# Kernel optimization log

Hardware: AMD Instinct MI355X
Metric: run time of the kernel (lower is better)

Reference implementation:

```python
import jax, jax.numpy as jnp
import numpy as np

F_DIM, H, O = 128, 256, 256
NQ, EQ = 64, 512
ND, ED = 50000, 600000

PARAM_SHAPES = [
    ("qW1", (F_DIM, H)), ("qb1", (H,)), ("qW2", (H, H)), ("qb2", (H,)),
    ("qW3", (H, H)),     ("qb3", (H,)), ("qW4", (H, O)), ("qb4", (O,)),
    ("dW1", (F_DIM, H)), ("db1", (H,)), ("dW2", (H, H)), ("db2", (H,)),
    ("dW3", (H, H)),     ("db3", (H,)), ("dW4", (H, O)), ("db4", (O,)),
    ("lW1", (2 * O, O)), ("lb1", (O,)),
    ("lW2", (O, O // 2)), ("lb2", (O // 2,)),
    ("lW3", (O // 2, 8)), ("lb3", (8,)),
]

def setup_inputs() -> dict:
    key = jax.random.key(0)
    ks = jax.random.split(key, 4 + len(PARAM_SHAPES))
    inp = {
        "query_in_feat": jax.random.normal(ks[0], (NQ, F_DIM), jnp.float32),
        "data_in_feat": jax.random.normal(ks[1], (ND, F_DIM), jnp.float32),
        "query_edge_list": jax.random.randint(ks[2], (2, EQ), 0, NQ),
        "data_edge_list": jax.random.randint(ks[3], (2, ED), 0, ND),
    }
    for i, (name, shape) in enumerate(PARAM_SHAPES):
        fan_in = shape[0] if len(shape) == 2 else 1
        inp[name] = jax.random.normal(ks[4 + i], shape, jnp.float32) * (1.0 / np.sqrt(fan_in))
    return inp

def _mlp2(x, W1, b1, W2, b2):
    return jnp.maximum(x @ W1 + b1, 0.0) @ W2 + b2

def _gin_conv(x, src, dst, W1, b1, W2, b2):
    # GINConv (eps=0): MLP(x_i + sum_{j->i} x_j); gather x[src], scatter-add at dst
    agg = jax.ops.segment_sum(x[src], dst, num_segments=x.shape[0])
    return _mlp2(x + agg, W1, b1, W2, b2)

def _gin(x, edge_index, p):
    src, dst = edge_index[0], edge_index[1]
    h = jnp.maximum(_gin_conv(x, src, dst, *p[:4]), 0.0)  # ReLU between convs
    return _gin_conv(h, src, dst, *p[4:])

def reference(query_in_feat, data_in_feat, query_edge_list, data_edge_list,
              qW1, qb1, qW2, qb2, qW3, qb3, qW4, qb4,
              dW1, db1, dW2, db2, dW3, db3, dW4, db4,
              lW1, lb1, lW2, lb2, lW3, lb3):
    qx = _gin(query_in_feat, query_edge_list, (qW1, qb1, qW2, qb2, qW3, qb3, qW4, qb4))
    dx = _gin(data_in_feat, data_edge_list, (dW1, db1, dW2, db2, dW3, db3, dW4, db4))
    # global_add_pool with batch = zeros -> single-graph sum
    qp = jnp.sum(qx, axis=0, keepdims=True)  # [1, O]
    dp = jnp.sum(dx, axis=0, keepdims=True)  # [1, O]
    h = jnp.concatenate([qp, dp], axis=1)    # [1, 2*O]
    h = jnp.maximum(h @ lW1 + lb1, 0.0)
    h = jnp.maximum(h @ lW2 + lb2, 0.0)
    h = jnp.maximum(h @ lW3 + lb3, 0.0)
    return h.reshape(1, 8)
```

## Files before the change

kernel.cpp:

```cpp
#include <hip/hip_runtime.h>
#include <hip/hip_bf16.h>


#define NQ 64
#define EQ 512
#define ND 50000
#define ED 600000
#define FDIM 128
#define HDIM 256
#define MLP_GRID 512

typedef __attribute__((ext_vector_type(8))) short short8;
typedef __attribute__((ext_vector_type(4))) float f32x4;
typedef __attribute__((ext_vector_type(2))) float floatx2;
typedef __attribute__((ext_vector_type(4))) unsigned short us4;
typedef __attribute__((ext_vector_type(2))) unsigned short us2;

__device__ __forceinline__ unsigned short f2bf(float f) {
    union { float f; unsigned u; } v; v.f = f;
    unsigned r = v.u + 0x7FFF + ((v.u >> 16) & 1);
    return (unsigned short)(r >> 16);
}
__device__ __forceinline__ float bf2f(unsigned short u) {
    union { unsigned u; float f; } v; v.u = ((unsigned)u) << 16;
    return v.f;
}


struct PackDesc {
    const float* W[8];
    unsigned short* Wp[8];
    int KT[8];
    int start[9];
};

__device__ __forceinline__ void pack_unit(const PackDesc& pd, int unit, int l) {
    int m = 0;
    while (m < 7 && unit >= pd.start[m + 1]) ++m;
    const int local = unit - pd.start[m];
    const int KT = pd.KT[m];
    const int kt = local % KT;
    const int ct = local / KT;
    const float* W = pd.W[m];
    unsigned short* Wp = pd.Wp[m];
    const int row = kt * 32 + (l >> 4) * 8;
    const int col = ct * 16 + (l & 15);
    short8 v;
#pragma unroll
    for (int j = 0; j < 8; ++j) v[j] = (short)f2bf(W[(size_t)(row + j) * 256 + col]);
    *(short8*)(Wp + (((size_t)(ct * KT + kt)) * 64 + l) * 8) = v;
}


__global__ void prepass(const float* __restrict__ xd, const float* __restrict__ xq,
                        unsigned char* __restrict__ x8, long long nd4, long long n4,
                        int cvt_b, PackDesc pd, int pack_units, int pack_b,
                        const int* __restrict__ d_dst, int* __restrict__ d_deg,
                        const int* __restrict__ q_dst, int* __restrict__ q_deg,
                        int d_eb) {
    const int b = blockIdx.x;
    const int tid = threadIdx.x;
    if (b < cvt_b) {
        long long i = (long long)b * 256 + tid;
        if (i >= n4) return;
        const float* src = (i < nd4) ? (xd + i * 4) : (xq + (i - nd4) * 4);
        float4 v = *(const float4*)src;
        int p = __builtin_amdgcn_cvt_pk_fp8_f32(v.x, v.y, 0, false);
        p = __builtin_amdgcn_cvt_pk_fp8_f32(v.z, v.w, p, true);
        *(unsigned*)(x8 + i * 4) = (unsigned)p;
    } else if (b < cvt_b + pack_b) {
        const int unit = (b - cvt_b) * 4 + (tid >> 6);
        if (unit < pack_units) pack_unit(pd, unit, tid & 63);
    } else {
        const int cb = b - cvt_b - pack_b;
        if (cb < d_eb) {
            int e = cb * 256 + tid;
            if (e < ED) atomicAdd(&d_deg[d_dst[e]], 1);
        } else {
            int e = (cb - d_eb) * 256 + tid;
            if (e < EQ) atomicAdd(&q_deg[q_dst[e]], 1);
        }
    }
}


__device__ __forceinline__ void scan1_body(const int* deg, int* rowptr, int* bsum,
                                           int n, int blk) {
    __shared__ int sh[256];
    const int t = threadIdx.x;
    const int i = blk * 256 + t;
    const int v = (i < n) ? deg[i] : 0;
    sh[t] = v;
    __syncthreads();
    for (int off = 1; off < 256; off <<= 1) {
        int x = (t >= off) ? sh[t - off] : 0;
        __syncthreads();
        sh[t] += x;
        __syncthreads();
    }
    if (i < n) rowptr[i] = sh[t] - v;
    if (t == 255) bsum[blk] = sh[255];
}

__global__ void scan_phase1_both(const int* __restrict__ d_deg, int* __restrict__ d_rowptr,
                                 int* __restrict__ d_bsum,
                                 const int* __restrict__ q_deg, int* __restrict__ q_rowptr,
                                 int* __restrict__ q_bsum, int dblocks) {
    int b = blockIdx.x;
    if (b < dblocks) scan1_body(d_deg, d_rowptr, d_bsum, ND, b);
    else             scan1_body(q_deg, q_rowptr, q_bsum, NQ, b - dblocks);
}

__device__ __forceinline__ void scan2_body(const int* bsum, int* boff, int* rowptr_n, int nb) {
    __shared__ int sh[256];
    const int t = threadIdx.x;
    const int v = (t < nb) ? bsum[t] : 0;
    sh[t] = v;
    __syncthreads();
    for (int off = 1; off < 256; off <<= 1) {
        int x = (t >= off) ? sh[t - off] : 0;
        __syncthreads();
        sh[t] += x;
        __syncthreads();
    }
    if (t < nb) boff[t] = sh[t] - v;
    if (t == 255) *rowptr_n = sh[255];
}

__global__ void scan_phase2_both(const int* __restrict__ d_bsum, int* __restrict__ d_boff,
                                 int* __restrict__ d_rowptr_n, int d_nb,
                                 const int* __restrict__ q_bsum, int* __restrict__ q_boff,
                                 int* __restrict__ q_rowptr_n, int q_nb) {
    if (blockIdx.x == 0) scan2_body(d_bsum, d_boff, d_rowptr_n, d_nb);
    else                 scan2_body(q_bsum, q_boff, q_rowptr_n, q_nb);
}

__global__ void scan_phase3_both(int* __restrict__ d_rowptr, const int* __restrict__ d_boff,
                                 int* __restrict__ d_cursor,
                                 int* __restrict__ q_rowptr, const int* __restrict__ q_boff,
                                 int* __restrict__ q_cursor, int dblocks) {
    int b = blockIdx.x;
    if (b < dblocks) {
        int i = b * 256 + threadIdx.x;
        if (i < ND) {
            int r = d_rowptr[i] + d_boff[b];
            d_rowptr[i] = r; d_cursor[i] = r;
        }
    } else {
        int i = (b - dblocks) * 256 + threadIdx.x;
        if (i < NQ) {
            int r = q_rowptr[i] + q_boff[b - dblocks];
            q_rowptr[i] = r; q_cursor[i] = r;
        }
    }
}

__global__ void fill_csr_both(const int* __restrict__ d_src, const int* __restrict__ d_dst,
                              int* __restrict__ d_cursor, int* __restrict__ d_csrsrc,
                              const int* __restrict__ q_src, const int* __restrict__ q_dst,
                              int* __restrict__ q_cursor, int* __restrict__ q_csrsrc,
                              int dblocks) {
    int b = blockIdx.x;
    if (b < dblocks) {
        int e = b * 256 + threadIdx.x;
        if (e < ED) {
            int p = atomicAdd(&d_cursor[d_dst[e]], 1);
            d_csrsrc[p] = d_src[e];
        }
    } else {
        int e = (b - dblocks) * 256 + threadIdx.x;
        if (e < EQ) {
            int p = atomicAdd(&q_cursor[q_dst[e]], 1);
            q_csrsrc[p] = q_src[e];
        }
    }
}


__global__ void gin_agg_f8_128_dual(const unsigned char* __restrict__ xd,
                                    const int* __restrict__ rpd, const int* __restrict__ csd,
                                    unsigned short* __restrict__ od,
                                    const unsigned char* __restrict__ xq,
                                    const int* __restrict__ rpq, const int* __restrict__ csq,
                                    unsigned short* __restrict__ oq, int ndpair) {
    const unsigned char* x; const int* rowptr; const int* csr; unsigned short* out; int nb;
    if ((int)blockIdx.x < ndpair) { x = xd; rowptr = rpd; csr = csd; out = od; nb = blockIdx.x; }
    else { x = xq; rowptr = rpq; csr = csq; out = oq; nb = blockIdx.x - ndpair; }

    const int t = threadIdx.x;
    const int node = nb * 2 + (t >> 5);
    const int c = t & 31;

    const int beg = rowptr[node];
    const int end = rowptr[node + 1];

    float a0, a1, a2, a3;
    {
        const unsigned w = *(const unsigned*)(x + (size_t)node * 128 + c * 4);
        floatx2 lo = __builtin_amdgcn_cvt_pk_f32_fp8((int)w, false);
        floatx2 hi = __builtin_amdgcn_cvt_pk_f32_fp8((int)w, true);
        a0 = lo[0]; a1 = lo[1]; a2 = hi[0]; a3 = hi[1];
    }
    for (int j = beg; j < end; ++j) {
        const unsigned w = *(const unsigned*)(x + (size_t)csr[j] * 128 + c * 4);
        floatx2 lo = __builtin_amdgcn_cvt_pk_f32_fp8((int)w, false);
        floatx2 hi = __builtin_amdgcn_cvt_pk_f32_fp8((int)w, true);
        a0 += lo[0]; a1 += lo[1]; a2 += hi[0]; a3 += hi[1];
    }
    us4 r;
    r[0] = f2bf(a0); r[1] = f2bf(a1); r[2] = f2bf(a2); r[3] = f2bf(a3);
    *(us4*)(out + (size_t)node * 128 + c * 4) = r;
}


__global__ void gin_agg_f8_256_dual(const unsigned char* __restrict__ xd,
                                    const int* __restrict__ rpd, const int* __restrict__ csd,
                                    unsigned short* __restrict__ od,
                                    const unsigned char* __restrict__ xq,
                                    const int* __restrict__ rpq, const int* __restrict__ csq,
                                    unsigned short* __restrict__ oq) {
    const unsigned char* x; const int* rowptr; const int* csr; unsigned short* out; int node;
    if ((int)blockIdx.x < ND) { x = xd; rowptr = rpd; csr = csd; out = od; node = blockIdx.x; }
    else { x = xq; rowptr = rpq; csr = csq; out = oq; node = blockIdx.x - ND; }

    const int t = threadIdx.x;
    const int beg = rowptr[node];
    const int end = rowptr[node + 1];

    float a0, a1, a2, a3;
    {
        const unsigned w = *(const unsigned*)(x + (size_t)node * 256 + t * 4);
        floatx2 lo = __builtin_amdgcn_cvt_pk_f32_fp8((int)w, false);
        floatx2 hi = __builtin_amdgcn_cvt_pk_f32_fp8((int)w, true);
        a0 = lo[0]; a1 = lo[1]; a2 = hi[0]; a3 = hi[1];
    }
    int j = beg;
    for (; j + 1 < end; j += 2) {
        const unsigned w0 = *(const unsigned*)(x + (size_t)csr[j] * 256 + t * 4);
        const unsigned w1 = *(const unsigned*)(x + (size_t)csr[j + 1] * 256 + t * 4);
        floatx2 l0 = __builtin_amdgcn_cvt_pk_f32_fp8((int)w0, false);
        floatx2 h0 = __builtin_amdgcn_cvt_pk_f32_fp8((int)w0, true);
        floatx2 l1 = __builtin_amdgcn_cvt_pk_f32_fp8((int)w1, false);
        floatx2 h1 = __builtin_amdgcn_cvt_pk_f32_fp8((int)w1, true);
        a0 += l0[0] + l1[0]; a1 += l0[1] + l1[1];
        a2 += h0[0] + h1[0]; a3 += h0[1] + h1[1];
    }
    if (j < end) {
        const unsigned w0 = *(const unsigned*)(x + (size_t)csr[j] * 256 + t * 4);
        floatx2 l0 = __builtin_amdgcn_cvt_pk_f32_fp8((int)w0, false);
        floatx2 h0 = __builtin_amdgcn_cvt_pk_f32_fp8((int)w0, true);
        a0 += l0[0]; a1 += l0[1]; a2 += h0[0]; a3 += h0[1];
    }
    us4 r;
    r[0] = f2bf(a0); r[1] = f2bf(a1); r[2] = f2bf(a2); r[3] = f2bf(a3);
    *(us4*)(out + (size_t)node * 256 + t * 4) = r;
}


template <int KIN>
__global__ __launch_bounds__(256) void mlp_dual(
    const unsigned short* __restrict__ Ad,
    const unsigned short* __restrict__ W1pd, const float* __restrict__ b1d,
    const unsigned short* __restrict__ W2pd, const float* __restrict__ b2d,
    unsigned char* __restrict__ C8d, float* __restrict__ poold, int ndtiles,
    const unsigned short* __restrict__ Aq,
    const unsigned short* __restrict__ W1pq, const float* __restrict__ b1q,
    const unsigned short* __restrict__ W2pq, const float* __restrict__ b2q,
    unsigned char* __restrict__ C8q, float* __restrict__ poolq,
    int relu_out, int total_tiles) {
    constexpr int KT1 = KIN / 32;
    constexpr int ISSUES = KIN / 32;
    constexpr int LPR = KIN / 8;
    constexpr int RPC = 1024 / (2 * KIN);
    __shared__ __align__(16) unsigned short lds[2][64 * 256];

    const int tid = threadIdx.x;
    const int lane = tid & 63;
    const int wv = tid >> 6;
    const int lrow = lane & 15;
    const int lk2 = (lane >> 4) * 8;

    const int nt = (total_tiles - (int)blockIdx.x + MLP_GRID - 1) / MLP_GRID;
    if (nt <= 0) return;

    const int rc = lane / LPR;
    const int cc = lane % LPR;

    auto STAGE = [&](int bu, int g) {
        const unsigned short* Abase =
            (g < ndtiles) ? (Ad + (size_t)g * 64 * KIN) : (Aq + (size_t)(g - ndtiles) * 64 * KIN);
#pragma unroll
        for (int i = 0; i < ISSUES; ++i) {
            const int chunk = wv * ISSUES + i;
            const int r = chunk * RPC + rc;
            const char* src = (const char*)Abase + (size_t)r * (2 * KIN) + ((cc ^ (r & 7)) << 4);
            __builtin_amdgcn_global_load_lds(src, (char*)&lds[bu][0] + chunk * 1024, 16, 0, 0);
        }
    };

    STAGE(0, (int)blockIdx.x);
    int cur = 0;

    for (int t = 0; t < nt; ++t) {
        const int g = (int)blockIdx.x + t * MLP_GRID;
        const unsigned short *W1p, *W2p; const float *b1, *b2;
        unsigned char* C8; float* pool; int row0, N;
        if (g < ndtiles) {
            W1p = W1pd; b1 = b1d; W2p = W2pd; b2 = b2d; C8 = C8d; pool = poold;
            row0 = g * 64; N = ND;
        } else {
            W1p = W1pq; b1 = b1q; W2p = W2pq; b2 = b2q; C8 = C8q; pool = poolq;
            row0 = (g - ndtiles) * 64; N = NQ;
        }

        __syncthreads();
        if (t + 1 < nt) STAGE(cur ^ 1, (int)blockIdx.x + (t + 1) * MLP_GRID);

        unsigned short* buf = &lds[cur][0];

        f32x4 acc1[4][4];
#pragma unroll
        for (int fm = 0; fm < 4; ++fm)
#pragma unroll
            for (int fn = 0; fn < 4; ++fn) acc1[fm][fn] = (f32x4)(0.f);

        const unsigned short* W1Base = W1p + ((size_t)(wv * 4) * KT1 * 64 + lane) * 8;
        for (int kt = 0; kt < KT1; ++kt) {
            short8 a[4], bf[4];
#pragma unroll
            for (int fm = 0; fm < 4; ++fm) {
                const int r = fm * 16 + lrow;
                unsigned byte = (unsigned)((r * KIN + kt * 32 + lk2) * 2) ^ (unsigned)((r & 7) << 4);
                a[fm] = *(const short8*)((const char*)buf + byte);
            }
#pragma unroll
            for (int fn = 0; fn < 4; ++fn)
                bf[fn] = *(const short8*)(W1Base + ((size_t)fn * KT1 + kt) * 64 * 8);
#pragma unroll
            for (int fm = 0; fm < 4; ++fm)
#pragma unroll
                for (int fn = 0; fn < 4; ++fn)
                    acc1[fm][fn] = __builtin_amdgcn_mfma_f32_16x16x32_bf16(
                        a[fm], bf[fn], acc1[fm][fn], 0, 0, 0);
        }
        __syncthreads();

#pragma unroll
        for (int fn = 0; fn < 4; ++fn) {
            const int col = wv * 64 + fn * 16 + lrow;
            const float bv = b1[col];
#pragma unroll
            for (int fm = 0; fm < 4; ++fm) {
                const int rbase = fm * 16 + (lane >> 4) * 4;
#pragma unroll
                for (int r = 0; r < 4; ++r) {
                    const int row = rbase + r;
                    const float v = fmaxf(acc1[fm][fn][r] + bv, 0.f);
                    unsigned byte = (unsigned)((row * 256 + col) * 2) ^ (unsigned)((row & 7) << 4);
                    *(unsigned short*)((char*)buf + byte) = f2bf(v);
                }
            }
        }
        __syncthreads();

        f32x4 acc2[4][4];
#pragma unroll
        for (int fm = 0; fm < 4; ++fm)
#pragma unroll
            for (int fn = 0; fn < 4; ++fn) acc2[fm][fn] = (f32x4)(0.f);

        const unsigned short* W2Base = W2p + ((size_t)(wv * 4) * 8 * 64 + lane) * 8;
        for (int kt = 0; kt < 8; ++kt) {
            short8 a[4], bf[4];
#pragma unroll
            for (int fm = 0; fm < 4; ++fm) {
                const int r = fm * 16 + lrow;
                unsigned byte = (unsigned)((r * 256 + kt * 32 + lk2) * 2) ^ (unsigned)((r & 7) << 4);
                a[fm] = *(const short8*)((const char*)buf + byte);
            }
#pragma unroll
            for (int fn = 0; fn < 4; ++fn)
                bf[fn] = *(const short8*)(W2Base + ((size_t)fn * 8 + kt) * 64 * 8);
#pragma unroll
            for (int fm = 0; fm < 4; ++fm)
#pragma unroll
                for (int fn = 0; fn < 4; ++fn)
                    acc2[fm][fn] = __builtin_amdgcn_mfma_f32_16x16x32_bf16(
                        a[fm], bf[fn], acc2[fm][fn], 0, 0, 0);
        }

#pragma unroll
        for (int fn = 0; fn < 4; ++fn) {
            const int col = wv * 64 + fn * 16 + lrow;
            const float bv = b2[col];
            float ps = 0.f;
#pragma unroll
            for (int fm = 0; fm < 4; ++fm) {
                const int rbase = row0 + fm * 16 + (lane >> 4) * 4;
#pragma unroll
                for (int r = 0; r < 4; ++r) {
                    const int row = rbase + r;
                    if (row < N) {
                        float v = acc2[fm][fn][r] + bv;
                        if (relu_out) v = fmaxf(v, 0.f);
                        if (C8) {
                            unsigned p = (unsigned)__builtin_amdgcn_cvt_pk_fp8_f32(v, v, 0, false);
                            C8[(size_t)row * 256 + col] = (unsigned char)(p & 0xff);
                        }
                        ps += v;
                    }
                }
            }
            if (pool) {
                ps += __shfl_xor(ps, 16);
                ps += __shfl_xor(ps, 32);
                if ((lane >> 4) == 0) atomicAdd(&pool[col], ps);
            }
        }
        cur ^= 1;
    }
}


__global__ void mlp_head(const float* __restrict__ pooled,
                         const float* __restrict__ lW1, const float* __restrict__ lb1,
                         const float* __restrict__ lW2, const float* __restrict__ lb2,
                         const float* __restrict__ lW3, const float* __restrict__ lb3,
                         float* __restrict__ out) {
    __shared__ float h0[512];
    __shared__ float h1[256];
    __shared__ float h2[128];
    const int t = threadIdx.x;
    h0[t] = pooled[t];
    h0[t + 256] = pooled[t + 256];
    __syncthreads();

    float acc = lb1[t];
    for (int k = 0; k < 512; ++k) acc += h0[k] * lW1[k * 256 + t];
    h1[t] = fmaxf(acc, 0.f);
    __syncthreads();

    if (t < 128) {
        float a = lb2[t];
        for (int k = 0; k < 256; ++k) a += h1[k] * lW2[k * 128 + t];
        h2[t] = fmaxf(a, 0.f);
    }
    __syncthreads();

    if (t < 8) {
        float a = lb3[t];
        for (int k = 0; k < 128; ++k) a += h2[k] * lW3[k * 8 + t];
        out[t] = fmaxf(a, 0.f);
    }
}


extern "C" void kernel_launch(void* const* d_in, const int* in_sizes, int n_in,
                              void* d_out, int out_size, void* d_ws, size_t ws_size,
                              hipStream_t stream) {
    const float* q_x  = (const float*)d_in[0];
    const float* d_x  = (const float*)d_in[1];
    const int*   q_el = (const int*)d_in[2];
    const int*   d_el = (const int*)d_in[3];
    const float* qW1 = (const float*)d_in[4];  const float* qb1 = (const float*)d_in[5];
    const float* qW2 = (const float*)d_in[6];  const float* qb2 = (const float*)d_in[7];
    const float* qW3 = (const float*)d_in[8];  const float* qb3 = (const float*)d_in[9];
    const float* qW4 = (const float*)d_in[10]; const float* qb4 = (const float*)d_in[11];
    const float* dW1 = (const float*)d_in[12]; const float* db1 = (const float*)d_in[13];
    const float* dW2 = (const float*)d_in[14]; const float* db2 = (const float*)d_in[15];
    const float* dW3 = (const float*)d_in[16]; const float* db3 = (const float*)d_in[17];
    const float* dW4 = (const float*)d_in[18]; const float* db4 = (const float*)d_in[19];
    const float* lW1 = (const float*)d_in[20]; const float* lb1 = (const float*)d_in[21];
    const float* lW2 = (const float*)d_in[22]; const float* lb2 = (const float*)d_in[23];
    const float* lW3 = (const float*)d_in[24]; const float* lb3 = (const float*)d_in[25];
    (void)in_sizes; (void)n_in; (void)out_size; (void)ws_size;

    const int* q_src = q_el;  const int* q_dst = q_el + EQ;
    const int* d_src = d_el;  const int* d_dst = d_el + ED;

    char* wsb = (char*)d_ws;
    size_t off = 0;
    auto alloc = [&](size_t bytes) { void* p = wsb + off; off += (bytes + 255) & ~(size_t)255; return p; };

    unsigned char*  x8d = (unsigned char*)alloc((size_t)ND * FDIM);
    unsigned char*  x8q = (unsigned char*)alloc((size_t)NQ * FDIM);
    unsigned short* dag = (unsigned short*)alloc((size_t)ND * FDIM * 2);
    unsigned short* qag = (unsigned short*)alloc((size_t)NQ * FDIM * 2);
    unsigned char*  h8d = (unsigned char*)alloc((size_t)ND * HDIM);
    unsigned char*  h8q = (unsigned char*)alloc((size_t)NQ * HDIM);
    unsigned short* had = (unsigned short*)alloc((size_t)ND * HDIM * 2);
    unsigned short* haq = (unsigned short*)alloc((size_t)NQ * HDIM * 2);
    float* pooled = (float*)alloc(512 * 4);
    int* d_deg    = (int*)alloc((size_t)ND * 4);
    int* q_deg    = (int*)alloc((size_t)NQ * 4);
    int* d_rowptr = (int*)alloc((size_t)(ND + 1) * 4);
    int* d_cursor = (int*)alloc((size_t)ND * 4);
    int* d_csrsrc = (int*)alloc((size_t)ED * 4);
    int* d_bsum   = (int*)alloc(256 * 4);
    int* d_boff   = (int*)alloc(256 * 4);
    int* q_rowptr = (int*)alloc((size_t)(NQ + 1) * 4);
    int* q_cursor = (int*)alloc((size_t)NQ * 4);
    int* q_csrsrc = (int*)alloc((size_t)EQ * 4);
    int* q_bsum   = (int*)alloc(256 * 4);
    int* q_boff   = (int*)alloc(256 * 4);
    unsigned short* pdW1 = (unsigned short*)alloc((size_t)FDIM * 256 * 2);
    unsigned short* pdW2 = (unsigned short*)alloc((size_t)HDIM * 256 * 2);
    unsigned short* pdW3 = (unsigned short*)alloc((size_t)HDIM * 256 * 2);
    unsigned short* pdW4 = (unsigned short*)alloc((size_t)HDIM * 256 * 2);
    unsigned short* pqW1 = (unsigned short*)alloc((size_t)FDIM * 256 * 2);
    unsigned short* pqW2 = (unsigned short*)alloc((size_t)HDIM * 256 * 2);
    unsigned short* pqW3 = (unsigned short*)alloc((size_t)HDIM * 256 * 2);
    unsigned short* pqW4 = (unsigned short*)alloc((size_t)HDIM * 256 * 2);

    hipMemsetAsync(pooled, 0, 512 * 4, stream);
    hipMemsetAsync(d_deg, 0, (char*)(q_deg + NQ) - (char*)d_deg, stream);

    const int d_eb = (ED + 255) / 256;
    const int q_eb = (EQ + 255) / 256;
    const int d_nb = (ND + 255) / 256;
    const int q_nb = (NQ + 255) / 256;
    {
        PackDesc pd;
        const float* Ws[8] = {dW1, dW2, dW3, dW4, qW1, qW2, qW3, qW4};
        unsigned short* Wps[8] = {pdW1, pdW2, pdW3, pdW4, pqW1, pqW2, pqW3, pqW4};
        int kts[8] = {4, 8, 8, 8, 4, 8, 8, 8};
        int s = 0;
        for (int i = 0; i < 8; ++i) {
            pd.W[i] = Ws[i]; pd.Wp[i] = Wps[i]; pd.KT[i] = kts[i];
            pd.start[i] = s; s += 16 * kts[i];
        }
        pd.start[8] = s;
        const int pack_units = s;
        const int pack_b = (s + 3) / 4;
        long long nd4 = (long long)ND * FDIM / 4;
        long long n4 = nd4 + (long long)NQ * FDIM / 4;
        const int cvt_b = (int)((n4 + 255) / 256);
        prepass<<<cvt_b + pack_b + d_eb + q_eb, 256, 0, stream>>>(
            d_x, q_x, x8d, nd4, n4, cvt_b, pd, pack_units, pack_b,
            d_dst, d_deg, q_dst, q_deg, d_eb);
    }

    scan_phase1_both<<<d_nb + q_nb, 256, 0, stream>>>(d_deg, d_rowptr, d_bsum,
                                                      q_deg, q_rowptr, q_bsum, d_nb);
    scan_phase2_both<<<2, 256, 0, stream>>>(d_bsum, d_boff, d_rowptr + ND, d_nb,
                                            q_bsum, q_boff, q_rowptr + NQ, q_nb);
    scan_phase3_both<<<d_nb + q_nb, 256, 0, stream>>>(d_rowptr, d_boff, d_cursor,
                                                      q_rowptr, q_boff, q_cursor, d_nb);
    fill_csr_both<<<d_eb + q_eb, 256, 0, stream>>>(d_src, d_dst, d_cursor, d_csrsrc,
                                                   q_src, q_dst, q_cursor, q_csrsrc, d_eb);

    const int ndpair = ND / 2;
    const int qpair = NQ / 2;
    const int ndtiles = (ND + 63) / 64;
    const int total_tiles = ndtiles + 1;

    gin_agg_f8_128_dual<<<ndpair + qpair, 64, 0, stream>>>(
        x8d, d_rowptr, d_csrsrc, dag, x8q, q_rowptr, q_csrsrc, qag, ndpair);
    mlp_dual<FDIM><<<MLP_GRID, 256, 0, stream>>>(
        dag, pdW1, db1, pdW2, db2, h8d, nullptr, ndtiles,
        qag, pqW1, qb1, pqW2, qb2, h8q, nullptr, 1, total_tiles);

    gin_agg_f8_256_dual<<<ND + NQ, 64, 0, stream>>>(
        h8d, d_rowptr, d_csrsrc, had, h8q, q_rowptr, q_csrsrc, haq);
    mlp_dual<HDIM><<<MLP_GRID, 256, 0, stream>>>(
        had, pdW3, db3, pdW4, db4, nullptr, pooled + 256, ndtiles,
        haq, pqW3, qb3, pqW4, qb4, nullptr, pooled, 0, total_tiles);

    mlp_head<<<1, 256, 0, stream>>>(pooled, lW1, lb1, lW2, lb2, lW3, lb3, (float*)d_out);
}
```

Before: 272.5 us.

## Split MLP into per-wave 16-row tiles with LDS pool reduction

Replaces the persistent 64-row-tile, double-buffered MLP kernel with a one-shot grid in which each wave independently processes a 16-row tile across all 256 output columns. The block-wide __syncthreads barriers between the two GEMM stages go away, and occupancy rises with launch_bounds(256,4) and a smaller LDS footprint. Pooled sums are reduced in shared memory before a single global atomic per column per block. In exchange, each wave streams the full weight matrices from cache for only 16 rows, so weight reuse per load drops about fourfold and global/L2 weight traffic grows. Prefetch overlap of the next tile is also lost.

```diff
diff --git a/kernel.cpp b/kernel.cpp
--- a/kernel.cpp
+++ b/kernel.cpp
@@ -8,7 +8,6 @@
 #define ED 600000
 #define FDIM 128
 #define HDIM 256
-#define MLP_GRID 512
 
 typedef __attribute__((ext_vector_type(8))) short short8;
 typedef __attribute__((ext_vector_type(4))) float f32x4;
@@ -258,11 +257,11 @@
 
 
 template <int KIN>
-__global__ __launch_bounds__(256) void mlp_dual(
+__global__ __launch_bounds__(256, 4) void mlp_dual(
     const unsigned short* __restrict__ Ad,
     const unsigned short* __restrict__ W1pd, const float* __restrict__ b1d,
     const unsigned short* __restrict__ W2pd, const float* __restrict__ b2d,
-    unsigned char* __restrict__ C8d, float* __restrict__ poold, int ndtiles,
+    unsigned char* __restrict__ C8d, float* __restrict__ poold, int ndt,
     const unsigned short* __restrict__ Aq,
     const unsigned short* __restrict__ W1pq, const float* __restrict__ b1q,
     const unsigned short* __restrict__ W2pq, const float* __restrict__ b2q,
@@ -272,7 +271,8 @@
     constexpr int ISSUES = KIN / 32;
     constexpr int LPR = KIN / 8;
     constexpr int RPC = 1024 / (2 * KIN);
-    __shared__ __align__(16) unsigned short lds[2][64 * 256];
+    __shared__ __align__(16) unsigned short lds[4][16 * 256];
+    __shared__ float poolsh[2][256];
 
     const int tid = threadIdx.x;
     const int lane = tid & 63;
@@ -280,144 +280,115 @@
     const int lrow = lane & 15;
     const int lk2 = (lane >> 4) * 8;
 
-    const int nt = (total_tiles - (int)blockIdx.x + MLP_GRID - 1) / MLP_GRID;
-    if (nt <= 0) return;
-
-    const int rc = lane / LPR;
-    const int cc = lane % LPR;
-
-    auto STAGE = [&](int bu, int g) {
-        const unsigned short* Abase =
-            (g < ndtiles) ? (Ad + (size_t)g * 64 * KIN) : (Aq + (size_t)(g - ndtiles) * 64 * KIN);
-#pragma unroll
-        for (int i = 0; i < ISSUES; ++i) {
-            const int chunk = wv * ISSUES + i;
-            const int r = chunk * RPC + rc;
-            const char* src = (const char*)Abase + (size_t)r * (2 * KIN) + ((cc ^ (r & 7)) << 4);
-            __builtin_amdgcn_global_load_lds(src, (char*)&lds[bu][0] + chunk * 1024, 16, 0, 0);
-        }
-    };
-
-    STAGE(0, (int)blockIdx.x);
-    int cur = 0;
-
-    for (int t = 0; t < nt; ++t) {
-        const int g = (int)blockIdx.x + t * MLP_GRID;
-        const unsigned short *W1p, *W2p; const float *b1, *b2;
-        unsigned char* C8; float* pool; int row0, N;
-        if (g < ndtiles) {
-            W1p = W1pd; b1 = b1d; W2p = W2pd; b2 = b2d; C8 = C8d; pool = poold;
-            row0 = g * 64; N = ND;
+    const bool do_pool = (poold != nullptr) || (poolq != nullptr);
+    if (do_pool) {
+        ((float*)poolsh)[tid] = 0.f;
+        ((float*)poolsh)[tid + 256] = 0.f;
+        __syncthreads();
+    }
+
+    const int g = (int)blockIdx.x * 4 + wv;
+    if (g < total_tiles) {
+        const unsigned short *A, *W1p, *W2p; const float *b1, *b2;
+        unsigned char* C8; int row0, graph;
+        if (g < ndt) {
+            A = Ad; W1p = W1pd; b1 = b1d; W2p = W2pd; b2 = b2d; C8 = C8d;
+            graph = 0; row0 = g * 16;
         } else {
-            W1p = W1pq; b1 = b1q; W2p = W2pq; b2 = b2q; C8 = C8q; pool = poolq;
-            row0 = (g - ndtiles) * 64; N = NQ;
-        }
-
-        __syncthreads();
-        if (t + 1 < nt) STAGE(cur ^ 1, (int)blockIdx.x + (t + 1) * MLP_GRID);
-
-        unsigned short* buf = &lds[cur][0];
-
-        f32x4 acc1[4][4];
-#pragma unroll
-        for (int fm = 0; fm < 4; ++fm)
-#pragma unroll
-            for (int fn = 0; fn < 4; ++fn) acc1[fm][fn] = (f32x4)(0.f);
-
-        const unsigned short* W1Base = W1p + ((size_t)(wv * 4) * KT1 * 64 + lane) * 8;
+            A = Aq; W1p = W1pq; b1 = b1q; W2p = W2pq; b2 = b2q; C8 = C8q;
+            graph = 1; row0 = (g - ndt) * 16;
+        }
+        unsigned short* slice = &lds[wv][0];
+
+        {
+            const char* Abase = (const char*)A + (size_t)row0 * KIN * 2;
+            const int rl = lane / LPR;
+            const int cc = lane % LPR;
+#pragma unroll
+            for (int i = 0; i < ISSUES; ++i) {
+                const int r = i * RPC + rl;
+                const char* src = Abase + (size_t)r * (2 * KIN) + ((size_t)(cc ^ (r & 7)) << 4);
+                __builtin_amdgcn_global_load_lds(src, (char*)slice + i * 1024, 16, 0, 0);
+            }
+        }
+        asm volatile("s_waitcnt vmcnt(0)" ::: "memory");
+
+        f32x4 acc1[16];
+#pragma unroll
+        for (int fn = 0; fn < 16; ++fn) acc1[fn] = (f32x4)(0.f);
+
         for (int kt = 0; kt < KT1; ++kt) {
-            short8 a[4], bf[4];
-#pragma unroll
-            for (int fm = 0; fm < 4; ++fm) {
-                const int r = fm * 16 + lrow;
-                unsigned byte = (unsigned)((r * KIN + kt * 32 + lk2) * 2) ^ (unsigned)((r & 7) << 4);
-                a[fm] = *(const short8*)((const char*)buf + byte);
+            const unsigned byte =
+                (unsigned)((lrow * KIN + kt * 32 + lk2) * 2) ^ (unsigned)((lrow & 7) << 4);
+            const short8 a = *(const short8*)((const char*)slice + byte);
+#pragma unroll
+            for (int fn = 0; fn < 16; ++fn) {
+                const short8 bf = *(const short8*)(W1p + (((size_t)(fn * KT1 + kt)) * 64 + lane) * 8);
+                acc1[fn] = __builtin_amdgcn_mfma_f32_16x16x32_bf16(a, bf, acc1[fn], 0, 0, 0);
             }
-#pragma unroll
-            for (int fn = 0; fn < 4; ++fn)
-                bf[fn] = *(const short8*)(W1Base + ((size_t)fn * KT1 + kt) * 64 * 8);
-#pragma unroll
-            for (int fm = 0; fm < 4; ++fm)
-#pragma unroll
-                for (int fn = 0; fn < 4; ++fn)
-                    acc1[fm][fn] = __builtin_amdgcn_mfma_f32_16x16x32_bf16(
-                        a[fm], bf[fn], acc1[fm][fn], 0, 0, 0);
-        }
-        __syncthreads();
-
-#pragma unroll
-        for (int fn = 0; fn < 4; ++fn) {
-            const int col = wv * 64 + fn * 16 + lrow;
+        }
+
+#pragma unroll
+        for (int fn = 0; fn < 16; ++fn) {
+            const int col = fn * 16 + lrow;
             const float bv = b1[col];
 #pragma unroll
-            for (int fm = 0; fm < 4; ++fm) {
-                const int rbase = fm * 16 + (lane >> 4) * 4;
-#pragma unroll
-                for (int r = 0; r < 4; ++r) {
-                    const int row = rbase + r;
-                    const float v = fmaxf(acc1[fm][fn][r] + bv, 0.f);
-                    unsigned byte = (unsigned)((row * 256 + col) * 2) ^ (unsigned)((row & 7) << 4);
-                    *(unsigned short*)((char*)buf + byte) = f2bf(v);
-                }
+            for (int r = 0; r < 4; ++r) {
+                const int row = (lane >> 4) * 4 + r;
+                const float v = fmaxf(acc1[fn][r] + bv, 0.f);
+                const unsigned byte =
+                    (unsigned)((row * 256 + col) * 2) ^ (unsigned)((row & 7) << 4);
+                *(unsigned short*)((char*)slice + byte) = f2bf(v);
             }
         }
-        __syncthreads();
-
-        f32x4 acc2[4][4];
-#pragma unroll
-        for (int fm = 0; fm < 4; ++fm)
-#pragma unroll
-            for (int fn = 0; fn < 4; ++fn) acc2[fm][fn] = (f32x4)(0.f);
-
-        const unsigned short* W2Base = W2p + ((size_t)(wv * 4) * 8 * 64 + lane) * 8;
+
+        f32x4 acc2[16];
+#pragma unroll
+        for (int fn = 0; fn < 16; ++fn) acc2[fn] = (f32x4)(0.f);
+
         for (int kt = 0; kt < 8; ++kt) {
-            short8 a[4], bf[4];
-#pragma unroll
-            for (int fm = 0; fm < 4; ++fm) {
-                const int r = fm * 16 + lrow;
-                unsigned byte = (unsigned)((r * 256 + kt * 32 + lk2) * 2) ^ (unsigned)((r & 7) << 4);
-                a[fm] = *(const short8*)((const char*)buf + byte);
+            const unsigned byte =
+                (unsigned)((lrow * 256 + kt * 32 + lk2) * 2) ^ (unsigned)((lrow & 7) << 4);
+            const short8 a = *(const short8*)((const char*)slice + byte);
+#pragma unroll
+            for (int fn = 0; fn < 16; ++fn) {
+                const short8 bf = *(const short8*)(W2p + (((size_t)(fn * 8 + kt)) * 64 + lane) * 8);
+                acc2[fn] = __builtin_amdgcn_mfma_f32_16x16x32_bf16(a, bf, acc2[fn], 0, 0, 0);
             }
-#pragma unroll
-            for (int fn = 0; fn < 4; ++fn)
-                bf[fn] = *(const short8*)(W2Base + ((size_t)fn * 8 + kt) * 64 * 8);
-#pragma unroll
-            for (int fm = 0; fm < 4; ++fm)
-#pragma unroll
-                for (int fn = 0; fn < 4; ++fn)
-                    acc2[fm][fn] = __builtin_amdgcn_mfma_f32_16x16x32_bf16(
-                        a[fm], bf[fn], acc2[fm][fn], 0, 0, 0);
-        }
-
-#pragma unroll
-        for (int fn = 0; fn < 4; ++fn) {
-            const int col = wv * 64 + fn * 16 + lrow;
+        }
+
+#pragma unroll
+        for (int fn = 0; fn < 16; ++fn) {
+            const int col = fn * 16 + lrow;
             const float bv = b2[col];
             float ps = 0.f;
 #pragma unroll
-            for (int fm = 0; fm < 4; ++fm) {
-                const int rbase = row0 + fm * 16 + (lane >> 4) * 4;
-#pragma unroll
-                for (int r = 0; r < 4; ++r) {
-                    const int row = rbase + r;
-                    if (row < N) {
-                        float v = acc2[fm][fn][r] + bv;
-                        if (relu_out) v = fmaxf(v, 0.f);
-                        if (C8) {
-                            unsigned p = (unsigned)__builtin_amdgcn_cvt_pk_fp8_f32(v, v, 0, false);
-                            C8[(size_t)row * 256 + col] = (unsigned char)(p & 0xff);
-                        }
-                        ps += v;
-                    }
+            for (int r = 0; r < 4; ++r) {
+                const int row = (lane >> 4) * 4 + r;
+                float v = acc2[fn][r] + bv;
+                if (relu_out) v = fmaxf(v, 0.f);
+                if (C8) {
+                    unsigned p = (unsigned)__builtin_amdgcn_cvt_pk_fp8_f32(v, v, 0, false);
+                    C8[(size_t)(row0 + row) * 256 + col] = (unsigned char)(p & 0xff);
                 }
+                ps += v;
             }
-            if (pool) {
+            if (do_pool) {
                 ps += __shfl_xor(ps, 16);
                 ps += __shfl_xor(ps, 32);
-                if ((lane >> 4) == 0) atomicAdd(&pool[col], ps);
+                if ((lane >> 4) == 0) atomicAdd(&poolsh[graph][col], ps);
             }
         }
-        cur ^= 1;
+    }
+
+    if (do_pool) {
+        __syncthreads();
+        const float vd = poolsh[0][tid & 255];
+        const float vq = poolsh[1][tid & 255];
+        if (tid < 256) {
+            if (poold && vd != 0.f) atomicAdd(&poold[tid], vd);
+            if (poolq && vq != 0.f) atomicAdd(&poolq[tid], vq);
+        }
     }
 }
 
@@ -551,19 +522,20 @@
 
     const int ndpair = ND / 2;
     const int qpair = NQ / 2;
-    const int ndtiles = (ND + 63) / 64;
-    const int total_tiles = ndtiles + 1;
+    const int ndt = ND / 16;
+    const int total_tiles = ndt + NQ / 16;
+    const int mlp_blocks = (total_tiles + 3) / 4;
 
     gin_agg_f8_128_dual<<<ndpair + qpair, 64, 0, stream>>>(
         x8d, d_rowptr, d_csrsrc, dag, x8q, q_rowptr, q_csrsrc, qag, ndpair);
-    mlp_dual<FDIM><<<MLP_GRID, 256, 0, stream>>>(
-        dag, pdW1, db1, pdW2, db2, h8d, nullptr, ndtiles,
+    mlp_dual<FDIM><<<mlp_blocks, 256, 0, stream>>>(
+        dag, pdW1, db1, pdW2, db2, h8d, nullptr, ndt,
         qag, pqW1, qb1, pqW2, qb2, h8q, nullptr, 1, total_tiles);
 
     gin_agg_f8_256_dual<<<ND + NQ, 64, 0, stream>>>(
         h8d, d_rowptr, d_csrsrc, had, h8q, q_rowptr, q_csrsrc, haq);
-    mlp_dual<HDIM><<<MLP_GRID, 256, 0, stream>>>(
-        had, pdW3, db3, pdW4, db4, nullptr, pooled + 256, ndtiles,
+    mlp_dual<HDIM><<<mlp_blocks, 256, 0, stream>>>(
+        had, pdW3, db3, pdW4, db4, nullptr, pooled + 256, ndt,
         haq, pqW3, qb3, pqW4, qb4, nullptr, pooled, 0, total_tiles);
 
     mlp_head<<<1, 256, 0, stream>>>(pooled, lW1, lb1, lW2, lb2, lW3, lb3, (float*)d_out);
```

Measured after the change: 388.4 us. 1.42x slower.
